# Kernel optimization log

Hardware: AMD Instinct MI355X
Metric: run time of the kernel (lower is better)

## Reference

```python
import jax, jax.numpy as jnp
import numpy as np

N_NODES = 50000


def gcn_conv(x, edge_index, edge_weight, W, b):
    """PyG GCNConv: h = x @ W.T; symmetric-norm aggregate with self loops; + bias."""
    n = x.shape[0]
    row, col = edge_index[0], edge_index[1]
    loop = jnp.arange(n)
    row_f = jnp.concatenate([row, loop])
    col_f = jnp.concatenate([col, loop])
    ew_f = jnp.concatenate([edge_weight, jnp.ones((n,), dtype=edge_weight.dtype)])
    # degree at destination (col), D^{-1/2} A D^{-1/2}
    deg = jax.ops.segment_sum(ew_f, col_f, num_segments=n)
    dinv = jnp.where(deg > 0, jax.lax.rsqrt(deg), 0.0)
    norm = dinv[row_f] * ew_f * dinv[col_f]  # [E+N]
    h = x @ W.T  # [N, out]
    msg = h[row_f] * norm[:, None]  # [E+N, out]
    out = jax.ops.segment_sum(msg, col_f, num_segments=n)
    return out + b


def prelu(x, alpha):
    return jnp.where(x >= 0, x, alpha[None, :] * x)


def setup_inputs() -> dict:
    key = jax.random.key(0)
    ks = jax.random.split(key, 8)
    in_c, hid, hid2, E = 512, 128, 64, 800000
    x = jax.random.normal(ks[0], (N_NODES, in_c), dtype=jnp.float32)
    edge_index = jax.random.randint(ks[1], (2, E), 0, N_NODES, dtype=jnp.int64)
    edge_weight = jax.random.uniform(ks[2], (E,), dtype=jnp.float32)
    s1 = 1.0 / np.sqrt(in_c)
    s2 = 1.0 / np.sqrt(hid)
    W1 = jax.random.uniform(ks[3], (hid, in_c), minval=-s1, maxval=s1, dtype=jnp.float32)
    b1 = jnp.zeros((hid,), dtype=jnp.float32)
    alpha1 = jnp.full((hid,), 0.25, dtype=jnp.float32)
    W2 = jax.random.uniform(ks[4], (hid2, hid), minval=-s2, maxval=s2, dtype=jnp.float32)
    b2 = jnp.zeros((hid2,), dtype=jnp.float32)
    alpha2 = jnp.full((hid2,), 0.25, dtype=jnp.float32)
    return {"x": x, "edge_index": edge_index, "edge_weight": edge_weight,
            "W1": W1, "b1": b1, "alpha1": alpha1,
            "W2": W2, "b2": b2, "alpha2": alpha2}


def reference(x, edge_index, edge_weight, W1, b1, alpha1, W2, b2, alpha2):
    h = gcn_conv(x, edge_index, edge_weight, W1, b1)
    h = prelu(h, alpha1)
    h = gcn_conv(h, edge_index, edge_weight, W2, b2)
    h = prelu(h, alpha2)
    return h
```

## Files before the change

### kernel.cpp

```cpp
#include <hip/hip_runtime.h>
#include <hip/hip_fp16.h>

#define IN_C 512
#define HID  128
#define HID2 64
#define CPAD 32

typedef __attribute__((ext_vector_type(8))) short short8v;
typedef __attribute__((ext_vector_type(4))) float float4v;

__device__ __forceinline__ unsigned short f2bf(float f) {
  unsigned u = __float_as_uint(f);
  unsigned r = u + 0x7FFF + ((u >> 16) & 1);
  return (unsigned short)(r >> 16);
}
__device__ __forceinline__ float bf2f(unsigned short h) {
  return __uint_as_float((unsigned)h << 16);
}
__device__ __forceinline__ uint2 pack4(unsigned short a, unsigned short b,
                                       unsigned short c, unsigned short d) {
  uint2 p;
  p.x = (unsigned)a | ((unsigned)b << 16);
  p.y = (unsigned)c | ((unsigned)d << 16);
  return p;
}

__global__ void k_detect(const unsigned* __restrict__ ei, int* __restrict__ flag) {
  __shared__ int nz;
  if (threadIdx.x == 0) nz = 0;
  __syncthreads();
  if (ei[2 * threadIdx.x + 1] != 0u) atomicOr(&nz, 1);
  __syncthreads();
  if (threadIdx.x == 0) *flag = (nz == 0) ? 1 : 0;
}

__device__ __forceinline__ int edge_at(const unsigned* __restrict__ ei, int f, int i) {
  return (int)(f ? ei[2 * (size_t)i] : ei[i]);
}

__global__ void k_cnt(const unsigned* __restrict__ ei, const int* __restrict__ flag,
                      int* __restrict__ cntp, int* __restrict__ rank, int E) {
  int f = *flag;
  int stride = gridDim.x * blockDim.x;
  for (int e = blockIdx.x * blockDim.x + threadIdx.x; e < E; e += stride) {
    int c = edge_at(ei, f, E + e);
    rank[e] = atomicAdd(&cntp[c * CPAD], 1);
  }
}

__global__ __launch_bounds__(256) void k_scanA(const int* __restrict__ cntp,
                                               int* __restrict__ part,
                                               int* __restrict__ bsum, int N) {
  __shared__ int tmp[256];
  int t = threadIdx.x;
  int idx = blockIdx.x * 1024 + t * 4;
  int4 v;
  v.x = idx + 0 < N ? cntp[(size_t)(idx + 0) * CPAD] : 0;
  v.y = idx + 1 < N ? cntp[(size_t)(idx + 1) * CPAD] : 0;
  v.z = idx + 2 < N ? cntp[(size_t)(idx + 2) * CPAD] : 0;
  v.w = idx + 3 < N ? cntp[(size_t)(idx + 3) * CPAD] : 0;
  int s = v.x + v.y + v.z + v.w;
  tmp[t] = s;
  __syncthreads();
#pragma unroll
  for (int d = 1; d < 256; d <<= 1) {
    int u = (t >= d) ? tmp[t - d] : 0;
    __syncthreads();
    tmp[t] += u;
    __syncthreads();
  }
  int excl = tmp[t] - s;
  int4 o;
  o.x = excl;
  o.y = excl + v.x;
  o.z = excl + v.x + v.y;
  o.w = excl + v.x + v.y + v.z;
  if (idx + 3 < N) {
    *(int4*)(part + idx) = o;
  } else {
    if (idx + 0 < N) part[idx + 0] = o.x;
    if (idx + 1 < N) part[idx + 1] = o.y;
    if (idx + 2 < N) part[idx + 2] = o.z;
    if (idx + 3 < N) part[idx + 3] = o.w;
  }
  if (t == 255) bsum[blockIdx.x] = tmp[255];
}

__global__ __launch_bounds__(256) void k_scanB(int* __restrict__ bsum, int nb) {
  __shared__ int tmp[256];
  int t = threadIdx.x;
  int s = (t < nb) ? bsum[t] : 0;
  tmp[t] = s;
  __syncthreads();
#pragma unroll
  for (int d = 1; d < 256; d <<= 1) {
    int u = (t >= d) ? tmp[t - d] : 0;
    __syncthreads();
    tmp[t] += u;
    __syncthreads();
  }
  bsum[t] = tmp[t] - s;
}

__global__ void k_scanC(const int* __restrict__ part, const int* __restrict__ bsum,
                        int* __restrict__ rowptr, int N, int E) {
  int i = blockIdx.x * blockDim.x + threadIdx.x;
  if (i < N) rowptr[i] = part[i] + bsum[i >> 10];
  if (i == 0) rowptr[N] = E;
}

__global__ void k_fill(const unsigned* __restrict__ ei, const int* __restrict__ flag,
                       const float* __restrict__ ew, const int* __restrict__ rowptr,
                       const int* __restrict__ rank, int* __restrict__ csrc,
                       float* __restrict__ cew, int E) {
  int f = *flag;
  int stride = gridDim.x * blockDim.x;
  for (int e = blockIdx.x * blockDim.x + threadIdx.x; e < E; e += stride) {
    int r = edge_at(ei, f, e);
    int c = edge_at(ei, f, E + e);
    int p = rowptr[c] + rank[e];
    csrc[p] = r;
    cew[p] = ew[e];
  }
}

__global__ void k_degsum(const float* __restrict__ cew, const int* __restrict__ rowptr,
                         float* __restrict__ dinv, int N) {
  int g = blockIdx.x * blockDim.x + threadIdx.x;
  int node = g >> 4, l = g & 15;
  if (node >= N) return;
  int s = rowptr[node], epd = rowptr[node + 1];
  float sum = 0.f;
  for (int p = s + l; p < epd; p += 16) sum += cew[p];
  sum += __shfl_xor(sum, 1);
  sum += __shfl_xor(sum, 2);
  sum += __shfl_xor(sum, 4);
  sum += __shfl_xor(sum, 8);
  if (l == 0) {
    float d = sum + 1.0f;
    float y = rsqrtf(d);
    y = y * (1.5f - 0.5f * d * y * y);
    dinv[node] = y;
  }
}

__global__ void k_scale(const int* __restrict__ csrc, const int* __restrict__ rowptr,
                        const float* __restrict__ dinv, float* __restrict__ cw, int N) {
  int g = blockIdx.x * blockDim.x + threadIdx.x;
  int node = g >> 4, l = g & 15;
  if (node >= N) return;
  float dn = dinv[node];
  int s = rowptr[node], epd = rowptr[node + 1];
  for (int p = s + l; p < epd; p += 16) cw[p] = dinv[csrc[p]] * cw[p] * dn;
}

__global__ __launch_bounds__(256) void k_gemm1m(const float* __restrict__ x,
                                                const float* __restrict__ W,
                                                __half* __restrict__ h, int M) {
  __shared__ short xh[4][128][8], xl[4][128][8];
  __shared__ short wh[4][128][8], wl[4][128][8];
  const int t = threadIdx.x;
  const int lane = t & 63, w = t >> 6;
  const int wm = (w >> 1) * 64, wn = (w & 1) * 64;
  const int kb = lane >> 4, r16 = lane & 15;
  const int m0 = blockIdx.x * 128;

  float4v acc[4][4];
#pragma unroll
  for (int mi = 0; mi < 4; mi++)
#pragma unroll
    for (int nj = 0; nj < 4; nj++) acc[mi][nj] = (float4v)0.f;

  for (int k0 = 0; k0 < IN_C; k0 += 32) {
#pragma unroll
    for (int i = 0; i < 4; i++) {
      int idx = t + i * 256;
      int row = idx >> 3, kc = idx & 7;
      int gr = m0 + row;
      if (gr >= M) gr = M - 1;
      float4 v = *(const float4*)(x + (size_t)gr * IN_C + k0 + kc * 4);
      unsigned short h0 = f2bf(v.x), h1 = f2bf(v.y), h2 = f2bf(v.z), h3 = f2bf(v.w);
      unsigned short l0 = f2bf(v.x - bf2f(h0)), l1 = f2bf(v.y - bf2f(h1));
      unsigned short l2 = f2bf(v.z - bf2f(h2)), l3 = f2bf(v.w - bf2f(h3));
      int kbw = kc >> 1, s = kc & 1;
      *(uint2*)&xh[kbw][row][s * 4] = pack4(h0, h1, h2, h3);
      *(uint2*)&xl[kbw][row][s * 4] = pack4(l0, l1, l2, l3);
    }
#pragma unroll
    for (int i = 0; i < 4; i++) {
      int idx = t + i * 256;
      int n = idx >> 3, kc = idx & 7;
      float4 v = *(const float4*)(W + (size_t)n * IN_C + k0 + kc * 4);
      unsigned short h0 = f2bf(v.x), h1 = f2bf(v.y), h2 = f2bf(v.z), h3 = f2bf(v.w);
      unsigned short l0 = f2bf(v.x - bf2f(h0)), l1 = f2bf(v.y - bf2f(h1));
      unsigned short l2 = f2bf(v.z - bf2f(h2)), l3 = f2bf(v.w - bf2f(h3));
      int kbw = kc >> 1, s = kc & 1;
      *(uint2*)&wh[kbw][n][s * 4] = pack4(h0, h1, h2, h3);
      *(uint2*)&wl[kbw][n][s * 4] = pack4(l0, l1, l2, l3);
    }
    __syncthreads();

    short8v ah[4], al[4], bh[4], bl[4];
#pragma unroll
    for (int mi = 0; mi < 4; mi++) {
      ah[mi] = *(short8v*)&xh[kb][wm + mi * 16 + r16][0];
      al[mi] = *(short8v*)&xl[kb][wm + mi * 16 + r16][0];
    }
#pragma unroll
    for (int nj = 0; nj < 4; nj++) {
      bh[nj] = *(short8v*)&wh[kb][wn + nj * 16 + r16][0];
      bl[nj] = *(short8v*)&wl[kb][wn + nj * 16 + r16][0];
    }
#pragma unroll
    for (int mi = 0; mi < 4; mi++)
#pragma unroll
      for (int nj = 0; nj < 4; nj++) {
        acc[mi][nj] = __builtin_amdgcn_mfma_f32_16x16x32_bf16(ah[mi], bh[nj], acc[mi][nj], 0, 0, 0);
        acc[mi][nj] = __builtin_amdgcn_mfma_f32_16x16x32_bf16(ah[mi], bl[nj], acc[mi][nj], 0, 0, 0);
        acc[mi][nj] = __builtin_amdgcn_mfma_f32_16x16x32_bf16(al[mi], bh[nj], acc[mi][nj], 0, 0, 0);
      }
    __syncthreads();
  }

#pragma unroll
  for (int mi = 0; mi < 4; mi++)
#pragma unroll
    for (int nj = 0; nj < 4; nj++) {
#pragma unroll
      for (int b = 0; b < 4; b++) {
        int grow = m0 + wm + mi * 16 + (lane >> 4) * 4 + b;
        int gcol = wn + nj * 16 + r16;
        if (grow < M) h[(size_t)grow * HID + gcol] = __float2half(acc[mi][nj][b]);
      }
    }
}

__global__ __launch_bounds__(256) void k_gemm2m(const float* __restrict__ z,
                                                const float* __restrict__ W,
                                                __half* __restrict__ h, int M) {
  __shared__ short zh[4][128][8], zl[4][128][8];
  __shared__ short wh[4][64][8], wl[4][64][8];
  const int t = threadIdx.x;
  const int lane = t & 63, w = t >> 6;
  const int wm = (w >> 1) * 64, wn = (w & 1) * 32;
  const int kb = lane >> 4, r16 = lane & 15;
  const int m0 = blockIdx.x * 128;

  float4v acc[4][2];
#pragma unroll
  for (int mi = 0; mi < 4; mi++)
#pragma unroll
    for (int nj = 0; nj < 2; nj++) acc[mi][nj] = (float4v)0.f;

  for (int k0 = 0; k0 < HID; k0 += 32) {
#pragma unroll
    for (int i = 0; i < 4; i++) {
      int idx = t + i * 256;
      int row = idx >> 3, kc = idx & 7;
      int gr = m0 + row;
      if (gr >= M) gr = M - 1;
      float4 v = *(const float4*)(z + (size_t)gr * HID + k0 + kc * 4);
      unsigned short h0 = f2bf(v.x), h1 = f2bf(v.y), h2 = f2bf(v.z), h3 = f2bf(v.w);
      unsigned short l0 = f2bf(v.x - bf2f(h0)), l1 = f2bf(v.y - bf2f(h1));
      unsigned short l2 = f2bf(v.z - bf2f(h2)), l3 = f2bf(v.w - bf2f(h3));
      int kbw = kc >> 1, s = kc & 1;
      *(uint2*)&zh[kbw][row][s * 4] = pack4(h0, h1, h2, h3);
      *(uint2*)&zl[kbw][row][s * 4] = pack4(l0, l1, l2, l3);
    }
#pragma unroll
    for (int i = 0; i < 2; i++) {
      int idx = t + i * 256;
      int n = idx >> 3, kc = idx & 7;
      float4 v = *(const float4*)(W + (size_t)n * HID + k0 + kc * 4);
      unsigned short h0 = f2bf(v.x), h1 = f2bf(v.y), h2 = f2bf(v.z), h3 = f2bf(v.w);
      unsigned short l0 = f2bf(v.x - bf2f(h0)), l1 = f2bf(v.y - bf2f(h1));
      unsigned short l2 = f2bf(v.z - bf2f(h2)), l3 = f2bf(v.w - bf2f(h3));
      int kbw = kc >> 1, s = kc & 1;
      *(uint2*)&wh[kbw][n][s * 4] = pack4(h0, h1, h2, h3);
      *(uint2*)&wl[kbw][n][s * 4] = pack4(l0, l1, l2, l3);
    }
    __syncthreads();

    short8v ah[4], al[4], bh[2], bl[2];
#pragma unroll
    for (int mi = 0; mi < 4; mi++) {
      ah[mi] = *(short8v*)&zh[kb][wm + mi * 16 + r16][0];
      al[mi] = *(short8v*)&zl[kb][wm + mi * 16 + r16][0];
    }
#pragma unroll
    for (int nj = 0; nj < 2; nj++) {
      bh[nj] = *(short8v*)&wh[kb][wn + nj * 16 + r16][0];
      bl[nj] = *(short8v*)&wl[kb][wn + nj * 16 + r16][0];
    }
#pragma unroll
    for (int mi = 0; mi < 4; mi++)
#pragma unroll
      for (int nj = 0; nj < 2; nj++) {
        acc[mi][nj] = __builtin_amdgcn_mfma_f32_16x16x32_bf16(ah[mi], bh[nj], acc[mi][nj], 0, 0, 0);
        acc[mi][nj] = __builtin_amdgcn_mfma_f32_16x16x32_bf16(ah[mi], bl[nj], acc[mi][nj], 0, 0, 0);
        acc[mi][nj] = __builtin_amdgcn_mfma_f32_16x16x32_bf16(al[mi], bh[nj], acc[mi][nj], 0, 0, 0);
      }
    __syncthreads();
  }

#pragma unroll
  for (int mi = 0; mi < 4; mi++)
#pragma unroll
    for (int nj = 0; nj < 2; nj++) {
#pragma unroll
      for (int b = 0; b < 4; b++) {
        int grow = m0 + wm + mi * 16 + (lane >> 4) * 4 + b;
        int gcol = wn + nj * 16 + r16;
        if (grow < M) h[(size_t)grow * HID2 + gcol] = __float2half(acc[mi][nj][b]);
      }
    }
}

__global__ void k_agg1(const __half* __restrict__ h, const int* __restrict__ rowptr,
                       const int* __restrict__ csrc, const float* __restrict__ cw,
                       const float* __restrict__ dinv, const float* __restrict__ bias,
                       const float* __restrict__ alpha, float* __restrict__ z, int N) {
  int node = blockIdx.x * 4 + (threadIdx.x >> 6);
  int lane = threadIdx.x & 63;
  if (node >= N) return;
  const __half2* hp = (const __half2*)h;
  float2 acc = make_float2(0.f, 0.f);
  int s = rowptr[node];
  int dg = rowptr[node + 1] - s;
  for (int base = 0; base < dg; base += 64) {
    int k = base + lane;
    int msrc = 0;
    float mw = 0.f;
    if (k < dg) {
      msrc = csrc[s + k];
      mw = cw[s + k];
    }
    int cnt = min(64, dg - base);
    for (int j = 0; j < cnt; j++) {
      int src = __shfl(msrc, j);
      float wv = __shfl(mw, j);
      float2 v = __half22float2(hp[(size_t)src * 64 + lane]);
      acc.x += wv * v.x;
      acc.y += wv * v.y;
    }
  }
  float di = dinv[node];
  float sw = di * di;
  float2 v = __half22float2(hp[(size_t)node * 64 + lane]);
  acc.x += sw * v.x;
  acc.y += sw * v.y;
  acc.x += bias[lane * 2];
  acc.y += bias[lane * 2 + 1];
  float a0 = alpha[lane * 2], a1 = alpha[lane * 2 + 1];
  acc.x = acc.x >= 0.f ? acc.x : a0 * acc.x;
  acc.y = acc.y >= 0.f ? acc.y : a1 * acc.y;
  ((float2*)z)[(size_t)node * 64 + lane] = acc;
}

__global__ void k_agg2(const __half* __restrict__ h, const int* __restrict__ rowptr,
                       const int* __restrict__ csrc, const float* __restrict__ cw,
                       const float* __restrict__ dinv, const float* __restrict__ bias,
                       const float* __restrict__ alpha, float* __restrict__ out, int N) {
  int node = blockIdx.x * 4 + (threadIdx.x >> 6);
  int lane = threadIdx.x & 63;
  if (node >= N) return;
  float acc = 0.f;
  int s = rowptr[node];
  int dg = rowptr[node + 1] - s;
  for (int base = 0; base < dg; base += 64) {
    int k = base + lane;
    int msrc = 0;
    float mw = 0.f;
    if (k < dg) {
      msrc = csrc[s + k];
      mw = cw[s + k];
    }
    int cnt = min(64, dg - base);
    for (int j = 0; j < cnt; j++) {
      int src = __shfl(msrc, j);
      float wv = __shfl(mw, j);
      acc += wv * __half2float(h[(size_t)src * HID2 + lane]);
    }
  }
  float di = dinv[node];
  acc += di * di * __half2float(h[(size_t)node * HID2 + lane]);
  acc += bias[lane];
  float a = alpha[lane];
  acc = acc >= 0.f ? acc : a * acc;
  out[(size_t)node * HID2 + lane] = acc;
}

extern "C" void kernel_launch(void* const* d_in, const int* in_sizes, int n_in,
                              void* d_out, int out_size, void* d_ws, size_t ws_size,
                              hipStream_t stream) {
  const float* x = (const float*)d_in[0];
  const unsigned* ei = (const unsigned*)d_in[1];
  const float* ew = (const float*)d_in[2];
  const float* W1 = (const float*)d_in[3];
  const float* b1 = (const float*)d_in[4];
  const float* a1 = (const float*)d_in[5];
  const float* W2 = (const float*)d_in[6];
  const float* b2 = (const float*)d_in[7];
  const float* a2 = (const float*)d_in[8];
  float* out = (float*)d_out;

  const int N = in_sizes[0] / IN_C;
  const int E = in_sizes[2];
  const int NB = (N + 1023) / 1024;

  char* w = (char*)d_ws;
  auto alloc = [&](size_t bytes) -> void* {
    void* p = (void*)w;
    w += (bytes + 255) / 256 * 256;
    return p;
  };
  int* flag = (int*)alloc(4);
  int* cntp = (int*)alloc((size_t)N * CPAD * 4);
  int* rank = (int*)alloc((size_t)E * 4);
  float* dinv = (float*)alloc((size_t)N * 4);
  int* rowptr = (int*)alloc((size_t)(N + 1) * 4);
  int* part = (int*)alloc((size_t)N * 4);
  int* bsum = (int*)alloc(256 * 4);
  int* csrc = (int*)alloc((size_t)E * 4);
  float* cw = (float*)alloc((size_t)E * 4);
  __half* h1 = (__half*)alloc((size_t)N * HID * 2);
  float* z1 = (float*)alloc((size_t)N * HID * 4);
  __half* h2 = (__half*)alloc((size_t)N * HID2 * 2);

  hipMemsetAsync(cntp, 0, (size_t)N * CPAD * 4, stream);

  k_detect<<<1, 256, 0, stream>>>(ei, flag);
  k_cnt<<<1024, 256, 0, stream>>>(ei, flag, cntp, rank, E);
  k_scanA<<<NB, 256, 0, stream>>>(cntp, part, bsum, N);
  k_scanB<<<1, 256, 0, stream>>>(bsum, NB);
  k_scanC<<<(N + 255) / 256, 256, 0, stream>>>(part, bsum, rowptr, N, E);
  k_fill<<<1024, 256, 0, stream>>>(ei, flag, ew, rowptr, rank, csrc, cw, E);
  k_degsum<<<(N * 16 + 255) / 256, 256, 0, stream>>>(cw, rowptr, dinv, N);
  k_scale<<<(N * 16 + 255) / 256, 256, 0, stream>>>(csrc, rowptr, dinv, cw, N);

  k_gemm1m<<<(N + 127) / 128, 256, 0, stream>>>(x, W1, h1, N);
  k_agg1<<<(N + 3) / 4, 256, 0, stream>>>(h1, rowptr, csrc, cw, dinv, b1, a1, z1, N);
  k_gemm2m<<<(N + 127) / 128, 256, 0, stream>>>(z1, W2, h2, N);
  k_agg2<<<(N + 3) / 4, 256, 0, stream>>>(h2, rowptr, csrc, cw, dinv, b2, a2, out, N);
}
```

Measured before the change: 393.1 us.

## Pre-split weights to bf16 hi/lo, pack CSR edges, vectorize edge counting

A new kernel converts W1 and W2 once into pre-laid-out bf16 hi/lo arrays, so the GEMM kernels no longer re-split the weights in every block. CSR source index and weight are interleaved into one uint2 array, so the aggregation and normalization kernels load both with a single access. k_cnt now handles two edges per thread with vector loads, and the aggregation inner loops are unrolled. Costs are an extra kernel launch and a little more workspace.

```diff
diff --git a/kernel.cpp b/kernel.cpp
--- a/kernel.cpp
+++ b/kernel.cpp
@@ -23,6 +23,13 @@
   p.x = (unsigned)a | ((unsigned)b << 16);
   p.y = (unsigned)c | ((unsigned)d << 16);
   return p;
+}
+__device__ __forceinline__ void split4(float4 v, uint2& hi, uint2& lo) {
+  unsigned short h0 = f2bf(v.x), h1 = f2bf(v.y), h2 = f2bf(v.z), h3 = f2bf(v.w);
+  unsigned short l0 = f2bf(v.x - bf2f(h0)), l1 = f2bf(v.y - bf2f(h1));
+  unsigned short l2 = f2bf(v.z - bf2f(h2)), l3 = f2bf(v.w - bf2f(h3));
+  hi = pack4(h0, h1, h2, h3);
+  lo = pack4(l0, l1, l2, l3);
 }
 
 __global__ void k_detect(const unsigned* __restrict__ ei, int* __restrict__ flag) {
@@ -38,13 +45,55 @@
   return (int)(f ? ei[2 * (size_t)i] : ei[i]);
 }
 
+__global__ void k_wsplit(const float* __restrict__ W1, const float* __restrict__ W2,
+                         short* __restrict__ w1h, short* __restrict__ w1l,
+                         short* __restrict__ w2h, short* __restrict__ w2l) {
+  int tid = blockIdx.x * blockDim.x + threadIdx.x;
+  if (tid < 128 * (IN_C / 4)) {
+    int n = tid >> 7, k = (tid & 127) * 4;
+    float4 v = *(const float4*)(W1 + (size_t)n * IN_C + k);
+    uint2 hi, lo;
+    split4(v, hi, lo);
+    size_t base = (((size_t)(k >> 3)) * 128 + n) * 8 + (k & 7);
+    *(uint2*)(w1h + base) = hi;
+    *(uint2*)(w1l + base) = lo;
+  } else if (tid < 128 * (IN_C / 4) + 64 * (HID / 4)) {
+    int t = tid - 128 * (IN_C / 4);
+    int n = t >> 5, k = (t & 31) * 4;
+    float4 v = *(const float4*)(W2 + (size_t)n * HID + k);
+    uint2 hi, lo;
+    split4(v, hi, lo);
+    size_t base = (((size_t)(k >> 3)) * 64 + n) * 8 + (k & 7);
+    *(uint2*)(w2h + base) = hi;
+    *(uint2*)(w2l + base) = lo;
+  }
+}
+
 __global__ void k_cnt(const unsigned* __restrict__ ei, const int* __restrict__ flag,
                       int* __restrict__ cntp, int* __restrict__ rank, int E) {
   int f = *flag;
-  int stride = gridDim.x * blockDim.x;
-  for (int e = blockIdx.x * blockDim.x + threadIdx.x; e < E; e += stride) {
-    int c = edge_at(ei, f, E + e);
-    rank[e] = atomicAdd(&cntp[c * CPAD], 1);
+  int stride = gridDim.x * blockDim.x * 2;
+  for (int e = (blockIdx.x * blockDim.x + threadIdx.x) * 2; e < E; e += stride) {
+    int c0, c1 = -1;
+    if (f) {
+      if (e + 1 < E) {
+        uint4 v = *(const uint4*)(ei + 2 * (size_t)(E + e));
+        c0 = (int)v.x;
+        c1 = (int)v.z;
+      } else {
+        c0 = (int)ei[2 * (size_t)(E + e)];
+      }
+    } else {
+      if (e + 1 < E) {
+        uint2 v = *(const uint2*)(ei + (size_t)E + e);
+        c0 = (int)v.x;
+        c1 = (int)v.y;
+      } else {
+        c0 = (int)ei[(size_t)E + e];
+      }
+    }
+    rank[e] = atomicAdd(&cntp[c0 * CPAD], 1);
+    if (c1 >= 0) rank[e + 1] = atomicAdd(&cntp[c1 * CPAD], 1);
   }
 }
 
@@ -111,27 +160,28 @@
 
 __global__ void k_fill(const unsigned* __restrict__ ei, const int* __restrict__ flag,
                        const float* __restrict__ ew, const int* __restrict__ rowptr,
-                       const int* __restrict__ rank, int* __restrict__ csrc,
-                       float* __restrict__ cew, int E) {
+                       const int* __restrict__ rank, uint2* __restrict__ ep, int E) {
   int f = *flag;
   int stride = gridDim.x * blockDim.x;
   for (int e = blockIdx.x * blockDim.x + threadIdx.x; e < E; e += stride) {
     int r = edge_at(ei, f, e);
     int c = edge_at(ei, f, E + e);
     int p = rowptr[c] + rank[e];
-    csrc[p] = r;
-    cew[p] = ew[e];
-  }
-}
-
-__global__ void k_degsum(const float* __restrict__ cew, const int* __restrict__ rowptr,
+    uint2 m;
+    m.x = (unsigned)r;
+    m.y = __float_as_uint(ew[e]);
+    ep[p] = m;
+  }
+}
+
+__global__ void k_degsum(const uint2* __restrict__ ep, const int* __restrict__ rowptr,
                          float* __restrict__ dinv, int N) {
   int g = blockIdx.x * blockDim.x + threadIdx.x;
   int node = g >> 4, l = g & 15;
   if (node >= N) return;
   int s = rowptr[node], epd = rowptr[node + 1];
   float sum = 0.f;
-  for (int p = s + l; p < epd; p += 16) sum += cew[p];
+  for (int p = s + l; p < epd; p += 16) sum += __uint_as_float(ep[p].y);
   sum += __shfl_xor(sum, 1);
   sum += __shfl_xor(sum, 2);
   sum += __shfl_xor(sum, 4);
@@ -144,18 +194,22 @@
   }
 }
 
-__global__ void k_scale(const int* __restrict__ csrc, const int* __restrict__ rowptr,
-                        const float* __restrict__ dinv, float* __restrict__ cw, int N) {
+__global__ void k_scale(uint2* __restrict__ ep, const int* __restrict__ rowptr,
+                        const float* __restrict__ dinv, int N) {
   int g = blockIdx.x * blockDim.x + threadIdx.x;
   int node = g >> 4, l = g & 15;
   if (node >= N) return;
   float dn = dinv[node];
   int s = rowptr[node], epd = rowptr[node + 1];
-  for (int p = s + l; p < epd; p += 16) cw[p] = dinv[csrc[p]] * cw[p] * dn;
+  for (int p = s + l; p < epd; p += 16) {
+    uint2 m = ep[p];
+    ep[p].y = __float_as_uint(dinv[m.x] * __uint_as_float(m.y) * dn);
+  }
 }
 
 __global__ __launch_bounds__(256) void k_gemm1m(const float* __restrict__ x,
-                                                const float* __restrict__ W,
+                                                const short* __restrict__ w1h,
+                                                const short* __restrict__ w1l,
                                                 __half* __restrict__ h, int M) {
   __shared__ short xh[4][128][8], xl[4][128][8];
   __shared__ short wh[4][128][8], wl[4][128][8];
@@ -179,24 +233,19 @@
       int gr = m0 + row;
       if (gr >= M) gr = M - 1;
       float4 v = *(const float4*)(x + (size_t)gr * IN_C + k0 + kc * 4);
-      unsigned short h0 = f2bf(v.x), h1 = f2bf(v.y), h2 = f2bf(v.z), h3 = f2bf(v.w);
-      unsigned short l0 = f2bf(v.x - bf2f(h0)), l1 = f2bf(v.y - bf2f(h1));
-      unsigned short l2 = f2bf(v.z - bf2f(h2)), l3 = f2bf(v.w - bf2f(h3));
+      uint2 hi, lo;
+      split4(v, hi, lo);
       int kbw = kc >> 1, s = kc & 1;
-      *(uint2*)&xh[kbw][row][s * 4] = pack4(h0, h1, h2, h3);
-      *(uint2*)&xl[kbw][row][s * 4] = pack4(l0, l1, l2, l3);
-    }
-#pragma unroll
-    for (int i = 0; i < 4; i++) {
+      *(uint2*)&xh[kbw][row][s * 4] = hi;
+      *(uint2*)&xl[kbw][row][s * 4] = lo;
+    }
+#pragma unroll
+    for (int i = 0; i < 2; i++) {
       int idx = t + i * 256;
-      int n = idx >> 3, kc = idx & 7;
-      float4 v = *(const float4*)(W + (size_t)n * IN_C + k0 + kc * 4);
-      unsigned short h0 = f2bf(v.x), h1 = f2bf(v.y), h2 = f2bf(v.z), h3 = f2bf(v.w);
-      unsigned short l0 = f2bf(v.x - bf2f(h0)), l1 = f2bf(v.y - bf2f(h1));
-      unsigned short l2 = f2bf(v.z - bf2f(h2)), l3 = f2bf(v.w - bf2f(h3));
-      int kbw = kc >> 1, s = kc & 1;
-      *(uint2*)&wh[kbw][n][s * 4] = pack4(h0, h1, h2, h3);
-      *(uint2*)&wl[kbw][n][s * 4] = pack4(l0, l1, l2, l3);
+      int kb2 = idx >> 7, n = idx & 127;
+      size_t gbase = (((size_t)(k0 >> 3) + kb2) * 128 + n) * 8;
+      *(short8v*)&wh[kb2][n][0] = *(const short8v*)(w1h + gbase);
+      *(short8v*)&wl[kb2][n][0] = *(const short8v*)(w1l + gbase);
     }
     __syncthreads();
 
@@ -236,7 +285,8 @@
 }
 
 __global__ __launch_bounds__(256) void k_gemm2m(const float* __restrict__ z,
-                                                const float* __restrict__ W,
+                                                const short* __restrict__ w2h,
+                                                const short* __restrict__ w2l,
                                                 __half* __restrict__ h, int M) {
   __shared__ short zh[4][128][8], zl[4][128][8];
   __shared__ short wh[4][64][8], wl[4][64][8];
@@ -260,24 +310,17 @@
       int gr = m0 + row;
       if (gr >= M) gr = M - 1;
       float4 v = *(const float4*)(z + (size_t)gr * HID + k0 + kc * 4);
-      unsigned short h0 = f2bf(v.x), h1 = f2bf(v.y), h2 = f2bf(v.z), h3 = f2bf(v.w);
-      unsigned short l0 = f2bf(v.x - bf2f(h0)), l1 = f2bf(v.y - bf2f(h1));
-      unsigned short l2 = f2bf(v.z - bf2f(h2)), l3 = f2bf(v.w - bf2f(h3));
+      uint2 hi, lo;
+      split4(v, hi, lo);
       int kbw = kc >> 1, s = kc & 1;
-      *(uint2*)&zh[kbw][row][s * 4] = pack4(h0, h1, h2, h3);
-      *(uint2*)&zl[kbw][row][s * 4] = pack4(l0, l1, l2, l3);
-    }
-#pragma unroll
-    for (int i = 0; i < 2; i++) {
-      int idx = t + i * 256;
-      int n = idx >> 3, kc = idx & 7;
-      float4 v = *(const float4*)(W + (size_t)n * HID + k0 + kc * 4);
-      unsigned short h0 = f2bf(v.x), h1 = f2bf(v.y), h2 = f2bf(v.z), h3 = f2bf(v.w);
-      unsigned short l0 = f2bf(v.x - bf2f(h0)), l1 = f2bf(v.y - bf2f(h1));
-      unsigned short l2 = f2bf(v.z - bf2f(h2)), l3 = f2bf(v.w - bf2f(h3));
-      int kbw = kc >> 1, s = kc & 1;
-      *(uint2*)&wh[kbw][n][s * 4] = pack4(h0, h1, h2, h3);
-      *(uint2*)&wl[kbw][n][s * 4] = pack4(l0, l1, l2, l3);
+      *(uint2*)&zh[kbw][row][s * 4] = hi;
+      *(uint2*)&zl[kbw][row][s * 4] = lo;
+    }
+    {
+      int kb2 = t >> 6, n = t & 63;
+      size_t gbase = (((size_t)(k0 >> 3) + kb2) * 64 + n) * 8;
+      *(short8v*)&wh[kb2][n][0] = *(const short8v*)(w2h + gbase);
+      *(short8v*)&wl[kb2][n][0] = *(const short8v*)(w2l + gbase);
     }
     __syncthreads();
 
@@ -317,9 +360,9 @@
 }
 
 __global__ void k_agg1(const __half* __restrict__ h, const int* __restrict__ rowptr,
-                       const int* __restrict__ csrc, const float* __restrict__ cw,
-                       const float* __restrict__ dinv, const float* __restrict__ bias,
-                       const float* __restrict__ alpha, float* __restrict__ z, int N) {
+                       const uint2* __restrict__ ep, const float* __restrict__ dinv,
+                       const float* __restrict__ bias, const float* __restrict__ alpha,
+                       float* __restrict__ z, int N) {
   int node = blockIdx.x * 4 + (threadIdx.x >> 6);
   int lane = threadIdx.x & 63;
   if (node >= N) return;
@@ -329,16 +372,13 @@
   int dg = rowptr[node + 1] - s;
   for (int base = 0; base < dg; base += 64) {
     int k = base + lane;
-    int msrc = 0;
-    float mw = 0.f;
-    if (k < dg) {
-      msrc = csrc[s + k];
-      mw = cw[s + k];
-    }
+    uint2 m = make_uint2(0u, 0u);
+    if (k < dg) m = ep[s + k];
     int cnt = min(64, dg - base);
+#pragma unroll 4
     for (int j = 0; j < cnt; j++) {
-      int src = __shfl(msrc, j);
-      float wv = __shfl(mw, j);
+      int src = __shfl((int)m.x, j);
+      float wv = __shfl(__uint_as_float(m.y), j);
       float2 v = __half22float2(hp[(size_t)src * 64 + lane]);
       acc.x += wv * v.x;
       acc.y += wv * v.y;
@@ -358,9 +398,9 @@
 }
 
 __global__ void k_agg2(const __half* __restrict__ h, const int* __restrict__ rowptr,
-                       const int* __restrict__ csrc, const float* __restrict__ cw,
-                       const float* __restrict__ dinv, const float* __restrict__ bias,
-                       const float* __restrict__ alpha, float* __restrict__ out, int N) {
+                       const uint2* __restrict__ ep, const float* __restrict__ dinv,
+                       const float* __restrict__ bias, const float* __restrict__ alpha,
+                       float* __restrict__ out, int N) {
   int node = blockIdx.x * 4 + (threadIdx.x >> 6);
   int lane = threadIdx.x & 63;
   if (node >= N) return;
@@ -369,16 +409,13 @@
   int dg = rowptr[node + 1] - s;
   for (int base = 0; base < dg; base += 64) {
     int k = base + lane;
-    int msrc = 0;
-    float mw = 0.f;
-    if (k < dg) {
-      msrc = csrc[s + k];
-      mw = cw[s + k];
-    }
+    uint2 m = make_uint2(0u, 0u);
+    if (k < dg) m = ep[s + k];
     int cnt = min(64, dg - base);
+#pragma unroll 4
     for (int j = 0; j < cnt; j++) {
-      int src = __shfl(msrc, j);
-      float wv = __shfl(mw, j);
+      int src = __shfl((int)m.x, j);
+      float wv = __shfl(__uint_as_float(m.y), j);
       acc += wv * __half2float(h[(size_t)src * HID2 + lane]);
     }
   }
@@ -421,8 +458,11 @@
   int* rowptr = (int*)alloc((size_t)(N + 1) * 4);
   int* part = (int*)alloc((size_t)N * 4);
   int* bsum = (int*)alloc(256 * 4);
-  int* csrc = (int*)alloc((size_t)E * 4);
-  float* cw = (float*)alloc((size_t)E * 4);
+  uint2* ep = (uint2*)alloc((size_t)E * 8);
+  short* w1h = (short*)alloc((size_t)HID * IN_C * 2);
+  short* w1l = (short*)alloc((size_t)HID * IN_C * 2);
+  short* w2h = (short*)alloc((size_t)HID2 * HID * 2);
+  short* w2l = (short*)alloc((size_t)HID2 * HID * 2);
   __half* h1 = (__half*)alloc((size_t)N * HID * 2);
   float* z1 = (float*)alloc((size_t)N * HID * 4);
   __half* h2 = (__half*)alloc((size_t)N * HID2 * 2);
@@ -430,16 +470,18 @@
   hipMemsetAsync(cntp, 0, (size_t)N * CPAD * 4, stream);
 
   k_detect<<<1, 256, 0, stream>>>(ei, flag);
+  k_wsplit<<<(128 * (IN_C / 4) + 64 * (HID / 4) + 255) / 256, 256, 0, stream>>>(
+      W1, W2, w1h, w1l, w2h, w2l);
   k_cnt<<<1024, 256, 0, stream>>>(ei, flag, cntp, rank, E);
   k_scanA<<<NB, 256, 0, stream>>>(cntp, part, bsum, N);
   k_scanB<<<1, 256, 0, stream>>>(bsum, NB);
   k_scanC<<<(N + 255) / 256, 256, 0, stream>>>(part, bsum, rowptr, N, E);
-  k_fill<<<1024, 256, 0, stream>>>(ei, flag, ew, rowptr, rank, csrc, cw, E);
-  k_degsum<<<(N * 16 + 255) / 256, 256, 0, stream>>>(cw, rowptr, dinv, N);
-  k_scale<<<(N * 16 + 255) / 256, 256, 0, stream>>>(csrc, rowptr, dinv, cw, N);
-
-  k_gemm1m<<<(N + 127) / 128, 256, 0, stream>>>(x, W1, h1, N);
-  k_agg1<<<(N + 3) / 4, 256, 0, stream>>>(h1, rowptr, csrc, cw, dinv, b1, a1, z1, N);
-  k_gemm2m<<<(N + 127) / 128, 256, 0, stream>>>(z1, W2, h2, N);
-  k_agg2<<<(N + 3) / 4, 256, 0, stream>>>(h2, rowptr, csrc, cw, dinv, b2, a2, out, N);
-}
+  k_fill<<<1024, 256, 0, stream>>>(ei, flag, ew, rowptr, rank, ep, E);
+  k_degsum<<<(N * 16 + 255) / 256, 256, 0, stream>>>(ep, rowptr, dinv, N);
+  k_scale<<<(N * 16 + 255) / 256, 256, 0, stream>>>(ep, rowptr, dinv, N);
+
+  k_gemm1m<<<(N + 127) / 128, 256, 0, stream>>>(x, w1h, w1l, h1, N);
+  k_agg1<<<(N + 3) / 4, 256, 0, stream>>>(h1, rowptr, ep, dinv, b1, a1, z1, N);
+  k_gemm2m<<<(N + 127) / 128, 256, 0, stream>>>(z1, w2h, w2l, h2, N);
+  k_agg2<<<(N + 3) / 4, 256, 0, stream>>>(h2, rowptr, ep, dinv, b2, a2, out, N);
+}
```

Result: faster. 374.7 us (-4.7%).
